# Performance work log

Hardware: AMD Instinct MI355X
Metric: run time of the kernel (lower is better)

The kernel has to match this reference:

```python
import jax, jax.numpy as jnp
import numpy as np

B, S, D = 8, 2048, 1024
N = 256          # state_dim
H = 512          # selector_hidden
E = 8            # num_experts


def murmurhash3_finalizer(token_ids):
    # Torch code works in int64 but masks to 32 bits after each multiply and
    # values stay non-negative, so it is exactly uint32 wrapping arithmetic.
    x = token_ids.astype(jnp.uint32)
    x = x ^ (x >> 16)
    x = x * jnp.uint32(2246822507)
    x = x ^ (x >> 13)
    x = x * jnp.uint32(3266489909)
    x = x ^ (x >> 16)
    return x


def setup_inputs() -> dict:
    key = jax.random.key(0)
    ks = jax.random.split(key, 7)
    scale = 0.02
    return {
        "x": jax.random.normal(ks[0], (B, S, D), dtype=jnp.float32),
        "token_ids": jax.random.randint(ks[1], (B, S), 0, 50257, dtype=jnp.int32),
        "Win": jax.random.normal(ks[2], (E, N, D), dtype=jnp.float32) * scale,      # in_proj.weight per expert
        "Wsin": jax.random.normal(ks[3], (E, H, D), dtype=jnp.float32) * scale,     # selector_in.weight
        "Wsout": jax.random.normal(ks[4], (E, 4 * N, H), dtype=jnp.float32) * scale,  # selector_out.weight
        "Wout": jax.random.normal(ks[5], (E, D, N), dtype=jnp.float32) * scale,     # out_proj.weight
        "dparam": jnp.ones((E, N), dtype=jnp.float32),                              # per-expert d
    }


def _forward(x, Win, Wsin, Wsout, Wout, dparam, token_ids):
    b, s, d = x.shape
    e_num, n, _ = Win.shape
    routes = (murmurhash3_finalizer(token_ids) % jnp.uint32(e_num)).astype(jnp.int32)  # (B,S)

    # Per-token expert projections, selected by hash route (masked accumulation
    # over the small fixed expert count; honors per-token routing).
    u = jnp.zeros((b, s, n), x.dtype)
    a = jnp.zeros((b, s, n), x.dtype)
    bg = jnp.zeros((b, s, n), x.dtype)
    c = jnp.zeros((b, s, n), x.dtype)
    dg = jnp.zeros((b, s, n), x.dtype)
    for e in range(e_num):
        m = (routes == e)[..., None]
        u = jnp.where(m, jnp.einsum('bsd,nd->bsn', x, Win[e]), u)
        sh = jax.nn.silu(jnp.einsum('bsd,hd->bsh', x, Wsin[e]))
        sel = jnp.einsum('bsh,oh->bso', sh, Wsout[e])       # (B,S,4N)
        ar, br, cr, dr = jnp.split(sel, 4, axis=-1)
        a = jnp.where(m, jax.nn.sigmoid(ar), a)
        bg = jnp.where(m, jnp.tanh(br), bg)
        c = jnp.where(m, jnp.tanh(cr), c)
        dg = jnp.where(m, jax.nn.sigmoid(dr), dg)

    dvec = dparam[routes]              # (B,S,N) expert d param per token
    skip = dvec * dg * u               # residual term, state-independent

    bidx = jnp.arange(b)

    def step(states, inp):
        # states: (B,E,N) per-expert hidden state per batch row
        route_t, u_t, a_t, b_t, c_t, skip_t = inp
        h_prev = states[bidx, route_t]                 # (B,N)
        h = a_t * h_prev + b_t * u_t
        states = states.at[bidx, route_t].set(h)       # only routed expert updates
        y = c_t * h + skip_t
        return states, y

    xs = (routes.swapaxes(0, 1), u.swapaxes(0, 1), a.swapaxes(0, 1),
          bg.swapaxes(0, 1), c.swapaxes(0, 1), skip.swapaxes(0, 1))
    states0 = jnp.zeros((b, e_num, n), x.dtype)
    _, ys = jax.lax.scan(step, states0, xs)            # ys: (S,B,N)
    y = ys.swapaxes(0, 1)                              # (B,S,N)

    out = jnp.zeros((b, s, d), x.dtype)
    for e in range(e_num):
        m = (routes == e)[..., None]
        out = jnp.where(m, jnp.einsum('bsn,dn->bsd', y, Wout[e]), out)
    return out


def reference(x, token_ids, Win, Wsin, Wsout, Wout, dparam):
    return _forward(x, Win, Wsin, Wsout, Wout, dparam, token_ids)
```

## Files before the change

kernel.cpp:

```cpp
#include <hip/hip_runtime.h>


#define TOKS 16384
#define RPAD 16512
#define DD   1024
#define NN   256
#define HH   512
#define MAXTILES  136
#define MAXCHUNKS 576
#define CHUNK 32
#define CVTBLKS 12288

typedef short short8 __attribute__((ext_vector_type(8)));
typedef float floatx4 __attribute__((ext_vector_type(4)));
typedef _Float16 half_t;

#define AS_GLOBAL __attribute__((address_space(1)))
#define AS_LDS    __attribute__((address_space(3)))

__device__ __forceinline__ void gl_lds16(const void* g, void* l) {
    __builtin_amdgcn_global_load_lds((const AS_GLOBAL void*)g, (AS_LDS void*)l, 16, 0, 0);
}

__device__ __forceinline__ unsigned short f2bf(float f) {
    union { float f; unsigned u; } c; c.f = f;
    unsigned r = c.u + 0x7FFF + ((c.u >> 16) & 1);
    return (unsigned short)(r >> 16);
}
__device__ __forceinline__ int route_of(int token) {
    unsigned x = (unsigned)token;
    x ^= x >> 16; x *= 2246822507u; x ^= x >> 13; x *= 3266489909u; x ^= x >> 16;
    return (int)(x & 7u);
}
__device__ __forceinline__ float sigm(float v) { return 1.0f / (1.0f + __expf(-v)); }
__device__ __forceinline__ float ftanh(float v) {
    float e = __expf(2.0f * v);
    return 1.0f - 2.0f / (e + 1.0f);
}

__global__ void k_route(const int* __restrict__ tok, int* __restrict__ cnt) {
    int b = blockIdx.x, tid = threadIdx.x;
    __shared__ int lc[256 * 8];
    #pragma unroll
    for (int e = 0; e < 8; e++) lc[tid * 8 + e] = 0;
    #pragma unroll
    for (int i = 0; i < 8; i++) {
        int e = route_of(tok[b * 2048 + tid * 8 + i]);
        lc[tid * 8 + e]++;
    }
    __syncthreads();
    if (tid < 8) {
        int s = 0;
        for (int t = 0; t < 256; t++) s += lc[t * 8 + tid];
        cnt[b * 8 + tid] = s;
    }
}

__global__ void k_offsets(const int* __restrict__ cnt, int* __restrict__ grpoff,
                          int* __restrict__ tileE, int* __restrict__ tileS,
                          int* __restrict__ tileR,
                          int* __restrict__ cGrp, int* __restrict__ cStart,
                          int* __restrict__ cLen, int* __restrict__ gBase,
                          int* __restrict__ meta) {
    __shared__ int sc[64], ce[8], eoff[9], etile[9], gb[65], go[64];
    int tid = threadIdx.x;
    if (tid < 64) sc[tid] = cnt[tid];
    __syncthreads();
    if (tid < 8) { int s = 0; for (int b = 0; b < 8; b++) s += sc[b * 8 + tid]; ce[tid] = s; }
    __syncthreads();
    if (tid == 0) {
        eoff[0] = 0; etile[0] = 0;
        for (int e = 0; e < 8; e++) {
            eoff[e + 1] = eoff[e] + ce[e];
            etile[e + 1] = etile[e] + (ce[e] + 127) / 128;
        }
        meta[0] = etile[8];
        gb[0] = 0;
        for (int g = 0; g < 64; g++) gb[g + 1] = gb[g] + (sc[g] + CHUNK - 1) / CHUNK;
        meta[1] = gb[64];
    }
    __syncthreads();
    if (tid < 64) {
        int b = tid >> 3, e = tid & 7;
        int run = eoff[e];
        for (int b2 = 0; b2 < b; b2++) run += sc[b2 * 8 + e];
        go[tid] = run;
        grpoff[tid] = run;
    }
    __syncthreads();
    if (tid < 8) {
        int e = tid, st = eoff[e], c = ce[e], t0 = etile[e];
        for (int i = 0, k = 0; i < c; i += 128, k++) {
            tileE[t0 + k] = e; tileS[t0 + k] = st + i;
            tileR[t0 + k] = (c - i < 128) ? (c - i) : 128;
        }
    }
    if (tid < 64) {
        int g = tid, n = sc[g], base = gb[g], s0 = go[g];
        gBase[g] = base;
        for (int i = 0, c = 0; i < n; i += CHUNK, c++) {
            cGrp[base + c] = g;
            cStart[base + c] = s0 + i;
            cLen[base + c] = (n - i < CHUNK) ? (n - i) : CHUNK;
        }
    }
}

__global__ void k_scatter(const int* __restrict__ tok, const int* __restrict__ grpoff,
                          int* __restrict__ perm) {
    int b = blockIdx.x, tid = threadIdx.x;
    int lane = tid & 63, w = tid >> 6;
    __shared__ unsigned wsum[4][4];
    int r[8];
    int myc[8] = {0,0,0,0,0,0,0,0};
    #pragma unroll
    for (int i = 0; i < 8; i++) {
        int e = route_of(tok[b * 2048 + tid * 8 + i]);
        r[i] = e; myc[e]++;
    }
    unsigned p[4], v[4];
    #pragma unroll
    for (int k = 0; k < 4; k++) {
        p[k] = (unsigned)myc[2 * k] | ((unsigned)myc[2 * k + 1] << 16);
        v[k] = p[k];
    }
    #pragma unroll
    for (int off = 1; off < 64; off <<= 1) {
        #pragma unroll
        for (int k = 0; k < 4; k++) {
            unsigned o = __shfl_up(v[k], off, 64);
            if (lane >= off) v[k] += o;
        }
    }
    if (lane == 63) {
        #pragma unroll
        for (int k = 0; k < 4; k++) wsum[w][k] = v[k];
    }
    __syncthreads();
    unsigned add[4] = {0, 0, 0, 0};
    for (int ww = 0; ww < w; ww++)
        #pragma unroll
        for (int k = 0; k < 4; k++) add[k] += wsum[ww][k];
    int basep[8];
    #pragma unroll
    for (int e = 0; e < 8; e++) {
        unsigned ex = v[e >> 1] + add[e >> 1] - p[e >> 1];
        basep[e] = grpoff[b * 8 + e] + (int)((e & 1) ? (ex >> 16) : (ex & 0xffffu));
    }
    #pragma unroll
    for (int i = 0; i < 8; i++) {
        int e = r[i];
        perm[basep[e]++] = b * 2048 + tid * 8 + i;
    }
}

__global__ void k_prep(const float* __restrict__ Win, const float* __restrict__ Wsin,
                       const float* __restrict__ Wsout, const float* __restrict__ Wout,
                       unsigned short* __restrict__ W12, unsigned short* __restrict__ Wso,
                       unsigned short* __restrict__ Wo,
                       const float* __restrict__ x, const int* __restrict__ perm,
                       unsigned short* __restrict__ Xs, unsigned short* __restrict__ SHb,
                       unsigned short* __restrict__ Yb) {
    int blk = blockIdx.x, tid = threadIdx.x;
    if (blk < CVTBLKS) {
        const int C12 = 8 * 768 * 1024 / 4, CSO = 8 * 1024 * 512 / 4;
        int c = blk * 256 + tid;
        floatx4 v; unsigned short* dst;
        if (c < C12) {
            int d = c * 4;
            int e = d / (768 * 1024);
            int rem = d - e * (768 * 1024);
            int r = rem >> 10, k = rem & 1023;
            const float* src = (r < 256) ? (Win + (((size_t)e * 256 + r) << 10) + k)
                                         : (Wsin + (((size_t)e * 512 + (r - 256)) << 10) + k);
            v = __builtin_nontemporal_load((const floatx4*)src);
            dst = W12 + d;
        } else if (c < C12 + CSO) {
            int d = (c - C12) * 4;
            v = __builtin_nontemporal_load((const floatx4*)(Wsout + d));
            dst = Wso + d;
        } else {
            int d = (c - C12 - CSO) * 4;
            v = __builtin_nontemporal_load((const floatx4*)(Wout + d));
            dst = Wo + d;
        }
        ushort4 o;
        o.x = f2bf(v[0]); o.y = f2bf(v[1]); o.z = f2bf(v[2]); o.w = f2bf(v[3]);
        *(ushort4*)dst = o;
    } else {
        int r = blk - CVTBLKS;
        if (r < TOKS) {
            int tok = perm[r];
            floatx4 v = __builtin_nontemporal_load(
                (const floatx4*)(x + (size_t)tok * 1024 + tid * 4));
            ushort4 o;
            o.x = f2bf(v[0]); o.y = f2bf(v[1]); o.z = f2bf(v[2]); o.w = f2bf(v[3]);
            *(ushort4*)(Xs + (size_t)r * 1024 + tid * 4) = o;
        } else {
            ushort4 z = {0, 0, 0, 0};
            *(ushort4*)(Xs + (size_t)r * 1024 + tid * 4) = z;
            if (tid < 128) *(ushort4*)(SHb + (size_t)r * 512 + tid * 4) = z;
            if (tid < 64)  *(ushort4*)(Yb + (size_t)r * 256 + tid * 4) = z;
        }
    }
}

template<int MODE, int KD>
__global__ __launch_bounds__(256, 4)
void k_mfma(const unsigned short* __restrict__ A, const unsigned short* __restrict__ Bw,
            const int* __restrict__ perm, const float* __restrict__ dparam,
            half_t* __restrict__ Ub, unsigned short* __restrict__ SHb,
            half_t* __restrict__ Aa, half_t* __restrict__ Wg,
            half_t* __restrict__ Cc, half_t* __restrict__ Sk,
            float* __restrict__ out,
            const int* __restrict__ tileE, const int* __restrict__ tileS,
            const int* __restrict__ tileR, const int* __restrict__ meta) {
    const int mt = blockIdx.x;
    if (mt >= meta[0]) return;
    const int e = tileE[mt], pos0 = tileS[mt], rows = tileR[mt];
    const int col0 = blockIdx.y * 64;
    const int tid = threadIdx.x;
    const int w = tid >> 6, lane = tid & 63, quad = lane >> 4, l15 = lane & 15;
    const int wm = w & 1, wn = w >> 1;
    constexpr int NOUT = (MODE == 0) ? 768 : 1024;
    constexpr int NK = KD / 32;

    __shared__ unsigned short As[3][128 * 32];
    __shared__ unsigned short Bs[3][64 * 32];

    const int r0 = tid >> 2;
    const int c8s = ((tid & 3) ^ ((tid >> 3) & 3)) * 8;
    const unsigned short* ga = A + (size_t)(pos0 + r0) * KD + c8s;
    const unsigned short* gb = Bw + ((size_t)e * NOUT + col0 + r0) * KD + c8s;

    const int sq = (quad ^ ((l15 >> 1) & 3)) * 8;
    int aoff[4], boff[2];
    #pragma unroll
    for (int i = 0; i < 4; i++) aoff[i] = (wm * 64 + i * 16 + l15) * 32 + sq;
    #pragma unroll
    for (int j = 0; j < 2; j++) boff[j] = (wn * 32 + j * 16 + l15) * 32 + sq;

    floatx4 acc[4][2] = {};

    #define STAGE(buf, k0) do { \
        gl_lds16(ga + (k0),                    As[buf] + w * 512); \
        gl_lds16(ga + (size_t)64 * KD + (k0),  As[buf] + 2048 + w * 512); \
        gl_lds16(gb + (k0),                    Bs[buf] + w * 512); \
    } while (0)

    STAGE(0, 0);
    STAGE(1, 32);
    int cur = 0, pre = 2;
    for (int kt = 0; kt < NK; kt++) {
        if (kt < NK - 1) {
            asm volatile("s_waitcnt vmcnt(3)" ::: "memory");
        } else {
            asm volatile("s_waitcnt vmcnt(0)" ::: "memory");
        }
        __builtin_amdgcn_s_barrier();
        asm volatile("" ::: "memory");
        if (kt + 2 < NK) STAGE(pre, (kt + 2) * 32);
        short8 af[4], bf[2];
        #pragma unroll
        for (int i = 0; i < 4; i++) af[i] = *(const short8*)(As[cur] + aoff[i]);
        #pragma unroll
        for (int j = 0; j < 2; j++) bf[j] = *(const short8*)(Bs[cur] + boff[j]);
        __builtin_amdgcn_s_setprio(1);
        #pragma unroll
        for (int i = 0; i < 4; i++)
            #pragma unroll
            for (int j = 0; j < 2; j++)
                acc[i][j] = __builtin_amdgcn_mfma_f32_16x16x32_bf16(af[i], bf[j], acc[i][j], 0, 0, 0);
        __builtin_amdgcn_s_setprio(0);
        asm volatile("s_waitcnt lgkmcnt(0)" ::: "memory");
        __builtin_amdgcn_sched_barrier(0);
        cur = (cur == 2) ? 0 : cur + 1;
        pre = (pre == 2) ? 0 : pre + 1;
    }
    #undef STAGE
    asm volatile("" ::: "memory");

    #pragma unroll
    for (int i = 0; i < 4; i++) {
        #pragma unroll
        for (int r = 0; r < 4; r++) {
            int m = wm * 64 + i * 16 + quad * 4 + r;
            if (m >= rows) continue;
            size_t row = (size_t)(pos0 + m);
            if (MODE == 0) {
                if (col0 < 256) {
                    #pragma unroll
                    for (int j = 0; j < 2; j++) {
                        int n = col0 + wn * 32 + j * 16 + l15;
                        Ub[row * 256 + n] = (half_t)acc[i][j][r];
                    }
                } else {
                    #pragma unroll
                    for (int j = 0; j < 2; j++) {
                        int n = col0 - 256 + wn * 32 + j * 16 + l15;
                        float v = acc[i][j][r];
                        SHb[row * 512 + n] = f2bf(v * sigm(v));
                    }
                }
            } else if (MODE == 1) {
                int region = col0 >> 8;
                #pragma unroll
                for (int j = 0; j < 2; j++) {
                    int n0 = (col0 & 255) + wn * 32 + j * 16 + l15;
                    size_t idx = row * 256 + (size_t)n0;
                    float v = acc[i][j][r];
                    if (region == 0) {
                        Aa[idx] = (half_t)sigm(v);
                    } else if (region == 1) {
                        Wg[idx] = (half_t)(ftanh(v) * (float)Ub[idx]);
                    } else if (region == 2) {
                        Cc[idx] = (half_t)ftanh(v);
                    } else {
                        Sk[idx] = (half_t)(dparam[e * 256 + n0] * sigm(v) * (float)Ub[idx]);
                    }
                }
            } else {
                int tok = perm[row];
                #pragma unroll
                for (int j = 0; j < 2; j++) {
                    int n = col0 + wn * 32 + j * 16 + l15;
                    __builtin_nontemporal_store(acc[i][j][r], &out[(size_t)tok * 1024 + n]);
                }
            }
        }
    }
}

__global__ void k_scanA(const half_t* __restrict__ Aa, const half_t* __restrict__ Wg,
                        const int* __restrict__ cStart, const int* __restrict__ cLen,
                        const int* __restrict__ meta,
                        float* __restrict__ SA, float* __restrict__ SQ) {
    int id = blockIdx.x;
    if (id >= meta[1]) return;
    int t = threadIdx.x;
    int s0 = cStart[id], L = cLen[id];
    size_t idx = (size_t)s0 * 256 + t;
    float p = 1.0f, q = 0.0f;
    if (L == CHUNK) {
        #pragma unroll
        for (int i = 0; i < CHUNK; i++) {
            float a = (float)Aa[idx + (size_t)i * 256], ww = (float)Wg[idx + (size_t)i * 256];
            q = a * q + ww;
            p *= a;
        }
    } else {
        for (int i = 0; i < L; i++) {
            float a = (float)Aa[idx], ww = (float)Wg[idx];
            q = a * q + ww;
            p *= a;
            idx += 256;
        }
    }
    SA[(size_t)id * 256 + t] = p;
    SQ[(size_t)id * 256 + t] = q;
}

__global__ void k_scanC(const half_t* __restrict__ Aa, const half_t* __restrict__ Wg,
                        const half_t* __restrict__ Cc, const half_t* __restrict__ Sk,
                        const int* __restrict__ cGrp, const int* __restrict__ cStart,
                        const int* __restrict__ cLen, const int* __restrict__ gBase,
                        const float* __restrict__ SA, const float* __restrict__ SQ,
                        const int* __restrict__ meta,
                        unsigned short* __restrict__ Yb) {
    int id = blockIdx.x;
    if (id >= meta[1]) return;
    int t = threadIdx.x;
    int g = cGrp[id];
    int base = gBase[g];
    int c = id - base;
    float h = 0.0f;
    for (int j = 0; j < c; j++) {
        size_t k = (size_t)(base + j) * 256 + t;
        h = SA[k] * h + SQ[k];
    }
    int s0 = cStart[id], L = cLen[id];
    size_t idx = (size_t)s0 * 256 + t;
    if (L == CHUNK) {
        #pragma unroll
        for (int i = 0; i < CHUNK; i++) {
            size_t k = idx + (size_t)i * 256;
            float a = (float)Aa[k], ww = (float)Wg[k];
            float cc = (float)Cc[k], sk = (float)Sk[k];
            h = a * h + ww;
            Yb[k] = f2bf(cc * h + sk);
        }
    } else {
        for (int i = 0; i < L; i++) {
            float a = (float)Aa[idx], ww = (float)Wg[idx];
            float cc = (float)Cc[idx], sk = (float)Sk[idx];
            h = a * h + ww;
            Yb[idx] = f2bf(cc * h + sk);
            idx += 256;
        }
    }
}

extern "C" void kernel_launch(void* const* d_in, const int* in_sizes, int n_in,
                              void* d_out, int out_size, void* d_ws, size_t ws_size,
                              hipStream_t stream) {
    const float* xin   = (const float*)d_in[0];
    const int*   tok   = (const int*)d_in[1];
    const float* Win   = (const float*)d_in[2];
    const float* Wsin  = (const float*)d_in[3];
    const float* Wsout = (const float*)d_in[4];
    const float* Wout  = (const float*)d_in[5];
    const float* dpar  = (const float*)d_in[6];
    float* out = (float*)d_out;

    size_t off = 0;
    char* base = (char*)d_ws;
    auto alloc = [&](size_t bytes) -> void* {
        void* p = base + off;
        off += (bytes + 255) & ~(size_t)255;
        return p;
    };
    half_t*         Ub  = (half_t*)alloc((size_t)RPAD * NN * 2);
    unsigned short* SHb = (unsigned short*)alloc((size_t)RPAD * HH * 2);
    unsigned short* Xs  = (unsigned short*)alloc((size_t)RPAD * DD * 2);
    unsigned short* Yb  = (unsigned short*)alloc((size_t)RPAD * NN * 2);
    half_t* Aa = (half_t*)alloc((size_t)TOKS * NN * 2);
    half_t* Wg = (half_t*)alloc((size_t)TOKS * NN * 2);
    half_t* Cc = (half_t*)alloc((size_t)TOKS * NN * 2);
    half_t* Sk = (half_t*)alloc((size_t)TOKS * NN * 2);
    unsigned short* W12 = (unsigned short*)alloc((size_t)8 * 768 * 1024 * 2);
    unsigned short* Wso = (unsigned short*)alloc((size_t)8 * 1024 * 512 * 2);
    unsigned short* Wo  = (unsigned short*)alloc((size_t)8 * 1024 * 256 * 2);
    float* SA  = (float*)alloc((size_t)MAXCHUNKS * 256 * 4);
    float* SQ  = (float*)alloc((size_t)MAXCHUNKS * 256 * 4);
    int* perm   = (int*)alloc(TOKS * 4);
    int* cnt    = (int*)alloc(64 * 4);
    int* grpoff = (int*)alloc(64 * 4);
    int* tileE  = (int*)alloc(MAXTILES * 4);
    int* tileS  = (int*)alloc(MAXTILES * 4);
    int* tileR  = (int*)alloc(MAXTILES * 4);
    int* cGrp   = (int*)alloc(MAXCHUNKS * 4);
    int* cStart = (int*)alloc(MAXCHUNKS * 4);
    int* cLen   = (int*)alloc(MAXCHUNKS * 4);
    int* gBase  = (int*)alloc(64 * 4);
    int* meta   = (int*)alloc(16 * 4);

    k_route<<<8, 256, 0, stream>>>(tok, cnt);
    k_offsets<<<1, 256, 0, stream>>>(cnt, grpoff, tileE, tileS, tileR,
                                     cGrp, cStart, cLen, gBase, meta);
    k_scatter<<<8, 256, 0, stream>>>(tok, grpoff, perm);
    k_prep<<<CVTBLKS + RPAD, 256, 0, stream>>>(Win, Wsin, Wsout, Wout, W12, Wso, Wo,
                                               xin, perm, Xs, SHb, Yb);

    k_mfma<0, 1024><<<dim3(MAXTILES, 12), 256, 0, stream>>>(Xs, W12, perm, dpar,
        Ub, SHb, Aa, Wg, Cc, Sk, out, tileE, tileS, tileR, meta);
    k_mfma<1, 512><<<dim3(MAXTILES, 16), 256, 0, stream>>>(SHb, Wso, perm, dpar,
        Ub, SHb, Aa, Wg, Cc, Sk, out, tileE, tileS, tileR, meta);

    k_scanA<<<MAXCHUNKS, 256, 0, stream>>>(Aa, Wg, cStart, cLen, meta, SA, SQ);
    k_scanC<<<MAXCHUNKS, 256, 0, stream>>>(Aa, Wg, Cc, Sk, cGrp, cStart, cLen,
                                           gBase, SA, SQ, meta, Yb);

    k_mfma<2, 256><<<dim3(MAXTILES, 16), 256, 0, stream>>>(Yb, Wo, perm, dpar,
        Ub, SHb, Aa, Wg, Cc, Sk, out, tileE, tileS, tileR, meta);
}
```

Baseline: 329.3 us.

## Make grouped GEMMs persistent with cross-tile prefetch and fold offsets into scatter

The three expert GEMM kernels now launch a fixed grid of 1024 blocks. Each block loops over several (row-tile, column-block) work items and keeps its 3-stage global-to-LDS pipeline running across tile boundaries, so the next tile's loads overlap the epilogue of the current one. The separate offsets kernel is merged into the scatter kernel, which recomputes the per-group prefix sums locally and saves one launch. In exchange the inner loop carries more control flow, and tiles are handed out in a strided order that may hurt L2 reuse of weights.

```diff
diff --git a/kernel.cpp b/kernel.cpp
--- a/kernel.cpp
+++ b/kernel.cpp
@@ -10,6 +10,7 @@
 #define MAXCHUNKS 576
 #define CHUNK 32
 #define CVTBLKS 12288
+#define GEMMGRID 1024
 
 typedef short short8 __attribute__((ext_vector_type(8)));
 typedef float floatx4 __attribute__((ext_vector_type(4)));
@@ -56,60 +57,16 @@
     }
 }
 
-__global__ void k_offsets(const int* __restrict__ cnt, int* __restrict__ grpoff,
+__global__ void k_scatter(const int* __restrict__ tok, const int* __restrict__ cnt,
+                          int* __restrict__ perm,
                           int* __restrict__ tileE, int* __restrict__ tileS,
                           int* __restrict__ tileR,
                           int* __restrict__ cGrp, int* __restrict__ cStart,
                           int* __restrict__ cLen, int* __restrict__ gBase,
                           int* __restrict__ meta) {
-    __shared__ int sc[64], ce[8], eoff[9], etile[9], gb[65], go[64];
-    int tid = threadIdx.x;
-    if (tid < 64) sc[tid] = cnt[tid];
-    __syncthreads();
-    if (tid < 8) { int s = 0; for (int b = 0; b < 8; b++) s += sc[b * 8 + tid]; ce[tid] = s; }
-    __syncthreads();
-    if (tid == 0) {
-        eoff[0] = 0; etile[0] = 0;
-        for (int e = 0; e < 8; e++) {
-            eoff[e + 1] = eoff[e] + ce[e];
-            etile[e + 1] = etile[e] + (ce[e] + 127) / 128;
-        }
-        meta[0] = etile[8];
-        gb[0] = 0;
-        for (int g = 0; g < 64; g++) gb[g + 1] = gb[g] + (sc[g] + CHUNK - 1) / CHUNK;
-        meta[1] = gb[64];
-    }
-    __syncthreads();
-    if (tid < 64) {
-        int b = tid >> 3, e = tid & 7;
-        int run = eoff[e];
-        for (int b2 = 0; b2 < b; b2++) run += sc[b2 * 8 + e];
-        go[tid] = run;
-        grpoff[tid] = run;
-    }
-    __syncthreads();
-    if (tid < 8) {
-        int e = tid, st = eoff[e], c = ce[e], t0 = etile[e];
-        for (int i = 0, k = 0; i < c; i += 128, k++) {
-            tileE[t0 + k] = e; tileS[t0 + k] = st + i;
-            tileR[t0 + k] = (c - i < 128) ? (c - i) : 128;
-        }
-    }
-    if (tid < 64) {
-        int g = tid, n = sc[g], base = gb[g], s0 = go[g];
-        gBase[g] = base;
-        for (int i = 0, c = 0; i < n; i += CHUNK, c++) {
-            cGrp[base + c] = g;
-            cStart[base + c] = s0 + i;
-            cLen[base + c] = (n - i < CHUNK) ? (n - i) : CHUNK;
-        }
-    }
-}
-
-__global__ void k_scatter(const int* __restrict__ tok, const int* __restrict__ grpoff,
-                          int* __restrict__ perm) {
     int b = blockIdx.x, tid = threadIdx.x;
     int lane = tid & 63, w = tid >> 6;
+    __shared__ int sc[64], eoff[9], etile[9], gbs[65];
     __shared__ unsigned wsum[4][4];
     int r[8];
     int myc[8] = {0,0,0,0,0,0,0,0};
@@ -118,6 +75,27 @@
         int e = route_of(tok[b * 2048 + tid * 8 + i]);
         r[i] = e; myc[e]++;
     }
+    if (tid < 64) sc[tid] = cnt[tid];
+    __syncthreads();
+    if (tid == 0) {
+        int ce[8];
+        for (int e = 0; e < 8; e++) {
+            int s = 0;
+            for (int b2 = 0; b2 < 8; b2++) s += sc[b2 * 8 + e];
+            ce[e] = s;
+        }
+        eoff[0] = 0;
+        for (int e = 0; e < 8; e++) eoff[e + 1] = eoff[e] + ce[e];
+        if (b == 0) {
+            etile[0] = 0;
+            for (int e = 0; e < 8; e++) etile[e + 1] = etile[e] + (ce[e] + 127) / 128;
+            meta[0] = etile[8];
+            gbs[0] = 0;
+            for (int g = 0; g < 64; g++) gbs[g + 1] = gbs[g] + (sc[g] + CHUNK - 1) / CHUNK;
+            meta[1] = gbs[64];
+        }
+    }
+    __syncthreads();
     unsigned p[4], v[4];
     #pragma unroll
     for (int k = 0; k < 4; k++) {
@@ -144,13 +122,36 @@
     int basep[8];
     #pragma unroll
     for (int e = 0; e < 8; e++) {
+        int run = eoff[e];
+        for (int b2 = 0; b2 < b; b2++) run += sc[b2 * 8 + e];
         unsigned ex = v[e >> 1] + add[e >> 1] - p[e >> 1];
-        basep[e] = grpoff[b * 8 + e] + (int)((e & 1) ? (ex >> 16) : (ex & 0xffffu));
+        basep[e] = run + (int)((e & 1) ? (ex >> 16) : (ex & 0xffffu));
     }
     #pragma unroll
     for (int i = 0; i < 8; i++) {
         int e = r[i];
         perm[basep[e]++] = b * 2048 + tid * 8 + i;
+    }
+    if (b == 0) {
+        if (tid < 8) {
+            int e = tid, st = eoff[e], c = eoff[e + 1] - eoff[e], t0 = etile[e];
+            for (int i = 0, k = 0; i < c; i += 128, k++) {
+                tileE[t0 + k] = e; tileS[t0 + k] = st + i;
+                tileR[t0 + k] = (c - i < 128) ? (c - i) : 128;
+            }
+        }
+        if (tid < 64) {
+            int g = tid, e = g & 7;
+            int n = sc[g], base = gbs[g];
+            int s0 = eoff[e];
+            for (int b2 = 0; b2 < (g >> 3); b2++) s0 += sc[b2 * 8 + e];
+            gBase[g] = base;
+            for (int i = 0, c = 0; i < n; i += CHUNK, c++) {
+                cGrp[base + c] = g;
+                cStart[base + c] = s0 + i;
+                cLen[base + c] = (n - i < CHUNK) ? (n - i) : CHUNK;
+            }
+        }
     }
 }
 
@@ -215,24 +216,26 @@
             float* __restrict__ out,
             const int* __restrict__ tileE, const int* __restrict__ tileS,
             const int* __restrict__ tileR, const int* __restrict__ meta) {
-    const int mt = blockIdx.x;
-    if (mt >= meta[0]) return;
-    const int e = tileE[mt], pos0 = tileS[mt], rows = tileR[mt];
-    const int col0 = blockIdx.y * 64;
+    constexpr int NOUT = (MODE == 0) ? 768 : 1024;
+    constexpr int NK = KD / 32;
+    constexpr int LNK = (NK == 32) ? 5 : (NK == 16) ? 4 : 3;
+    constexpr int NYB = (MODE == 0) ? 12 : 16;
+    const int meta0 = meta[0];
+    const int NT = meta0 * NYB;
+    const int G = gridDim.x;
+    const int bid = blockIdx.x;
+    if (bid >= NT) return;
+    const int nmine = (NT - 1 - bid) / G + 1;
+
     const int tid = threadIdx.x;
     const int w = tid >> 6, lane = tid & 63, quad = lane >> 4, l15 = lane & 15;
     const int wm = w & 1, wn = w >> 1;
-    constexpr int NOUT = (MODE == 0) ? 768 : 1024;
-    constexpr int NK = KD / 32;
 
     __shared__ unsigned short As[3][128 * 32];
     __shared__ unsigned short Bs[3][64 * 32];
 
     const int r0 = tid >> 2;
     const int c8s = ((tid & 3) ^ ((tid >> 3) & 3)) * 8;
-    const unsigned short* ga = A + (size_t)(pos0 + r0) * KD + c8s;
-    const unsigned short* gb = Bw + ((size_t)e * NOUT + col0 + r0) * KD + c8s;
-
     const int sq = (quad ^ ((l15 >> 1) & 3)) * 8;
     int aoff[4], boff[2];
     #pragma unroll
@@ -240,26 +243,49 @@
     #pragma unroll
     for (int j = 0; j < 2; j++) boff[j] = (wn * 32 + j * 16 + l15) * 32 + sq;
 
+    const unsigned short *gaS, *gbS;
+    int sTile = 0;
+    auto setS = [&](int k) {
+        int ti = bid + k * G;
+        int mt = ti % meta0, cb = ti / meta0;
+        gaS = A + (size_t)(tileS[mt] + r0) * KD + c8s;
+        gbS = Bw + ((size_t)tileE[mt] * NOUT + cb * 64 + r0) * KD + c8s;
+    };
+    int e_c, pos0_c, rows_c, col0_c, cIdx = 0;
+    auto setC = [&](int k) {
+        int ti = bid + k * G;
+        int mt = ti % meta0, cb = ti / meta0;
+        e_c = tileE[mt]; pos0_c = tileS[mt]; rows_c = tileR[mt]; col0_c = cb * 64;
+    };
+    setS(0); setC(0);
+
     floatx4 acc[4][2] = {};
 
     #define STAGE(buf, k0) do { \
-        gl_lds16(ga + (k0),                    As[buf] + w * 512); \
-        gl_lds16(ga + (size_t)64 * KD + (k0),  As[buf] + 2048 + w * 512); \
-        gl_lds16(gb + (k0),                    Bs[buf] + w * 512); \
+        gl_lds16(gaS + (k0),                    As[buf] + w * 512); \
+        gl_lds16(gaS + (size_t)64 * KD + (k0),  As[buf] + 2048 + w * 512); \
+        gl_lds16(gbS + (k0),                    Bs[buf] + w * 512); \
     } while (0)
 
     STAGE(0, 0);
     STAGE(1, 32);
     int cur = 0, pre = 2;
-    for (int kt = 0; kt < NK; kt++) {
-        if (kt < NK - 1) {
+    const int totalSteps = nmine * NK;
+    for (int c = 0; c < totalSteps; c++) {
+        if (c < totalSteps - 1) {
             asm volatile("s_waitcnt vmcnt(3)" ::: "memory");
         } else {
             asm volatile("s_waitcnt vmcnt(0)" ::: "memory");
         }
         __builtin_amdgcn_s_barrier();
         asm volatile("" ::: "memory");
-        if (kt + 2 < NK) STAGE(pre, (kt + 2) * 32);
+        const int sg = c + 2;
+        const bool boundary = ((c & (NK - 1)) == NK - 1);
+        if (!boundary && sg < totalSteps) {
+            int st = sg >> LNK;
+            if (st != sTile) { sTile = st; setS(st); }
+            STAGE(pre, (sg & (NK - 1)) * 32);
+        }
         short8 af[4], bf[2];
         #pragma unroll
         for (int i = 0; i < 4; i++) af[i] = *(const short8*)(As[cur] + aoff[i]);
@@ -274,61 +300,73 @@
         __builtin_amdgcn_s_setprio(0);
         asm volatile("s_waitcnt lgkmcnt(0)" ::: "memory");
         __builtin_amdgcn_sched_barrier(0);
+        if (boundary) {
+            #pragma unroll
+            for (int i = 0; i < 4; i++) {
+                #pragma unroll
+                for (int r = 0; r < 4; r++) {
+                    int m = wm * 64 + i * 16 + quad * 4 + r;
+                    if (m >= rows_c) continue;
+                    size_t row = (size_t)(pos0_c + m);
+                    if (MODE == 0) {
+                        if (col0_c < 256) {
+                            #pragma unroll
+                            for (int j = 0; j < 2; j++) {
+                                int n = col0_c + wn * 32 + j * 16 + l15;
+                                Ub[row * 256 + n] = (half_t)acc[i][j][r];
+                            }
+                        } else {
+                            #pragma unroll
+                            for (int j = 0; j < 2; j++) {
+                                int n = col0_c - 256 + wn * 32 + j * 16 + l15;
+                                float v = acc[i][j][r];
+                                SHb[row * 512 + n] = f2bf(v * sigm(v));
+                            }
+                        }
+                    } else if (MODE == 1) {
+                        int region = col0_c >> 8;
+                        #pragma unroll
+                        for (int j = 0; j < 2; j++) {
+                            int n0 = (col0_c & 255) + wn * 32 + j * 16 + l15;
+                            size_t idx = row * 256 + (size_t)n0;
+                            float v = acc[i][j][r];
+                            if (region == 0) {
+                                Aa[idx] = (half_t)sigm(v);
+                            } else if (region == 1) {
+                                Wg[idx] = (half_t)(ftanh(v) * (float)Ub[idx]);
+                            } else if (region == 2) {
+                                Cc[idx] = (half_t)ftanh(v);
+                            } else {
+                                Sk[idx] = (half_t)(dparam[e_c * 256 + n0] * sigm(v) * (float)Ub[idx]);
+                            }
+                        }
+                    } else {
+                        int tok = perm[row];
+                        #pragma unroll
+                        for (int j = 0; j < 2; j++) {
+                            int n = col0_c + wn * 32 + j * 16 + l15;
+                            __builtin_nontemporal_store(acc[i][j][r], &out[(size_t)tok * 1024 + n]);
+                        }
+                    }
+                }
+            }
+            #pragma unroll
+            for (int i = 0; i < 4; i++)
+                #pragma unroll
+                for (int j = 0; j < 2; j++)
+                    acc[i][j] = (floatx4){0.0f, 0.0f, 0.0f, 0.0f};
+            cIdx++;
+            if (cIdx < nmine) setC(cIdx);
+            if (sg < totalSteps) {
+                int st = sg >> LNK;
+                if (st != sTile) { sTile = st; setS(st); }
+                STAGE(pre, (sg & (NK - 1)) * 32);
+            }
+        }
         cur = (cur == 2) ? 0 : cur + 1;
         pre = (pre == 2) ? 0 : pre + 1;
     }
     #undef STAGE
-    asm volatile("" ::: "memory");
-
-    #pragma unroll
-    for (int i = 0; i < 4; i++) {
-        #pragma unroll
-        for (int r = 0; r < 4; r++) {
-            int m = wm * 64 + i * 16 + quad * 4 + r;
-            if (m >= rows) continue;
-            size_t row = (size_t)(pos0 + m);
-            if (MODE == 0) {
-                if (col0 < 256) {
-                    #pragma unroll
-                    for (int j = 0; j < 2; j++) {
-                        int n = col0 + wn * 32 + j * 16 + l15;
-                        Ub[row * 256 + n] = (half_t)acc[i][j][r];
-                    }
-                } else {
-                    #pragma unroll
-                    for (int j = 0; j < 2; j++) {
-                        int n = col0 - 256 + wn * 32 + j * 16 + l15;
-                        float v = acc[i][j][r];
-                        SHb[row * 512 + n] = f2bf(v * sigm(v));
-                    }
-                }
-            } else if (MODE == 1) {
-                int region = col0 >> 8;
-                #pragma unroll
-                for (int j = 0; j < 2; j++) {
-                    int n0 = (col0 & 255) + wn * 32 + j * 16 + l15;
-                    size_t idx = row * 256 + (size_t)n0;
-                    float v = acc[i][j][r];
-                    if (region == 0) {
-                        Aa[idx] = (half_t)sigm(v);
-                    } else if (region == 1) {
-                        Wg[idx] = (half_t)(ftanh(v) * (float)Ub[idx]);
-                    } else if (region == 2) {
-                        Cc[idx] = (half_t)ftanh(v);
-                    } else {
-                        Sk[idx] = (half_t)(dparam[e * 256 + n0] * sigm(v) * (float)Ub[idx]);
-                    }
-                }
-            } else {
-                int tok = perm[row];
-                #pragma unroll
-                for (int j = 0; j < 2; j++) {
-                    int n = col0 + wn * 32 + j * 16 + l15;
-                    __builtin_nontemporal_store(acc[i][j][r], &out[(size_t)tok * 1024 + n]);
-                }
-            }
-        }
-    }
 }
 
 __global__ void k_scanA(const half_t* __restrict__ Aa, const half_t* __restrict__ Wg,
@@ -434,7 +472,6 @@
     float* SQ  = (float*)alloc((size_t)MAXCHUNKS * 256 * 4);
     int* perm   = (int*)alloc(TOKS * 4);
     int* cnt    = (int*)alloc(64 * 4);
-    int* grpoff = (int*)alloc(64 * 4);
     int* tileE  = (int*)alloc(MAXTILES * 4);
     int* tileS  = (int*)alloc(MAXTILES * 4);
     int* tileR  = (int*)alloc(MAXTILES * 4);
@@ -445,21 +482,20 @@
     int* meta   = (int*)alloc(16 * 4);
 
     k_route<<<8, 256, 0, stream>>>(tok, cnt);
-    k_offsets<<<1, 256, 0, stream>>>(cnt, grpoff, tileE, tileS, tileR,
+    k_scatter<<<8, 256, 0, stream>>>(tok, cnt, perm, tileE, tileS, tileR,
                                      cGrp, cStart, cLen, gBase, meta);
-    k_scatter<<<8, 256, 0, stream>>>(tok, grpoff, perm);
     k_prep<<<CVTBLKS + RPAD, 256, 0, stream>>>(Win, Wsin, Wsout, Wout, W12, Wso, Wo,
                                                xin, perm, Xs, SHb, Yb);
 
-    k_mfma<0, 1024><<<dim3(MAXTILES, 12), 256, 0, stream>>>(Xs, W12, perm, dpar,
+    k_mfma<0, 1024><<<GEMMGRID, 256, 0, stream>>>(Xs, W12, perm, dpar,
         Ub, SHb, Aa, Wg, Cc, Sk, out, tileE, tileS, tileR, meta);
-    k_mfma<1, 512><<<dim3(MAXTILES, 16), 256, 0, stream>>>(SHb, Wso, perm, dpar,
+    k_mfma<1, 512><<<GEMMGRID, 256, 0, stream>>>(SHb, Wso, perm, dpar,
         Ub, SHb, Aa, Wg, Cc, Sk, out, tileE, tileS, tileR, meta);
 
     k_scanA<<<MAXCHUNKS, 256, 0, stream>>>(Aa, Wg, cStart, cLen, meta, SA, SQ);
     k_scanC<<<MAXCHUNKS, 256, 0, stream>>>(Aa, Wg, Cc, Sk, cGrp, cStart, cLen,
                                            gBase, SA, SQ, meta, Yb);
 
-    k_mfma<2, 256><<<dim3(MAXTILES, 16), 256, 0, stream>>>(Yb, Wo, perm, dpar,
+    k_mfma<2, 256><<<GEMMGRID, 256, 0, stream>>>(Yb, Wo, perm, dpar,
         Ub, SHb, Aa, Wg, Cc, Sk, out, tileE, tileS, tileR, meta);
 }
```

New measurement: 343.2 us. 4.2% more time.
